# Optimization experiments

Hardware: AMD Instinct MI355X
Metric: run time of the kernel (lower is better)

## Reference

```python
import jax, jax.numpy as jnp
import numpy as np

B, NQ, ISIZE = 8, 2048, 1024
H, D, NA = 8, 128, 8            # num_head, attn_dim, num_anchor
AH = H * D                      # ahsize = 1024
ASZ = NA * D                    # anchor_size = 1024
FH = 4096                       # _fhsize
ISZ_NET = FH * H // NA          # 4096, input dim of self.net
EPS = 1e-6


def setup_inputs() -> dict:
    key = jax.random.key(0)
    ks = jax.random.split(key, 12)
    def u(k, shape, fan_in):
        s = 1.0 / np.sqrt(fan_in)
        return jax.random.uniform(k, shape, jnp.float32, -s, s)
    return {
        "inputs": jax.random.normal(ks[0], (B, NQ, ISIZE), jnp.float32),
        "ln_g": jnp.ones((ISIZE,), jnp.float32),
        "ln_b": jnp.zeros((ISIZE,), jnp.float32),
        "q_anchor": u(ks[1], (H, NA, D), D),
        "W_qkv": u(ks[2], (ISIZE, 3 * AH), ISIZE), "b_qkv": jnp.zeros((3 * AH,), jnp.float32),
        "W_an": u(ks[3], (ASZ, FH), ASZ), "b_an": jnp.zeros((FH,), jnp.float32),
        "W_n1": u(ks[4], (ISZ_NET, AH), ISZ_NET), "b_n1": jnp.zeros((AH,), jnp.float32),
        "W_n2": u(ks[5], (AH, FH), AH), "b_n2": jnp.zeros((FH,), jnp.float32),
        "W_n3": u(ks[6], (FH, AH), FH), "b_n3": jnp.zeros((AH,), jnp.float32),
        "W_k": u(ks[7], (AH, AH), AH), "b_k": jnp.zeros((AH,), jnp.float32),
        "W_o": u(ks[8], (AH, ISIZE), AH), "b_o": jnp.zeros((ISIZE,), jnp.float32),
    }


def reference(inputs, ln_g, ln_b, q_anchor, W_qkv, b_qkv, W_an, b_an,
              W_n1, b_n1, W_n2, b_n2, W_n3, b_n3, W_k, b_k, W_o, b_o):
    b, nq = inputs.shape[:2]
    scale = 1.0 / np.sqrt(D)
    # pre-LayerNorm
    mu = jnp.mean(inputs, -1, keepdims=True)
    var = jnp.mean(jnp.square(inputs - mu), -1, keepdims=True)
    x = (inputs - mu) * jax.lax.rsqrt(var + EPS) * ln_g + ln_b
    # QKV projection
    qkv = (x @ W_qkv + b_qkv).reshape(b, nq, 3, H, D)
    q = jnp.transpose(qkv[:, :, 0], (0, 2, 1, 3))   # [b,H,nq,D]
    k = qkv[:, :, 1]                                  # [b,nq,H,D]
    v = qkv[:, :, 2]                                  # [b,nq,H,D]
    # stage 1: fixed anchors attend over the sequence
    sc1 = jax.nn.softmax(jnp.einsum('had,bnhd->bhan', q_anchor, k) * scale, axis=-1)
    out = jnp.einsum('bhan,bnhd->bhad', sc1, v).reshape(b, H, ASZ)   # [b,H,NA*D]
    # anchor_net (share_head Linear + ReLU)
    out = jax.nn.relu(out @ W_an + b_an)                              # [b,H,FH]
    # regroup head-major -> anchor-major
    out = out.reshape(b, H, NA, FH // NA).transpose(0, 2, 1, 3).reshape(b, NA, ISZ_NET)
    # net: bottleneck Linear -> Linear -> ReLU -> Linear
    out = jax.nn.relu((out @ W_n1 + b_n1) @ W_n2 + b_n2) @ W_n3 + b_n3  # [b,NA,AH]
    # stage 2: queries attend over anchors
    kk = (out @ W_k + b_k).reshape(b, NA, H, D)
    sc2 = jax.nn.softmax(jnp.einsum('bhqd,bahd->bhqa', q, kk) * scale, axis=-1)
    ov = out.reshape(b, NA, H, D)
    y = jnp.einsum('bhqa,bahd->bqhd', sc2, ov).reshape(b, nq, AH)
    return y @ W_o + b_o + inputs
```

## Files before the change

### kernel.cpp

```cpp
#include <hip/hip_runtime.h>
#include <cstdint>
#include <cstddef>

typedef unsigned short u16;
typedef __attribute__((ext_vector_type(8))) short short8;
typedef __attribute__((ext_vector_type(4))) float floatx4;

__device__ __forceinline__ u16 f2bf(float f) {
  unsigned u = __float_as_uint(f);
  u += 0x7fffu + ((u >> 16) & 1u);
  return (u16)(u >> 16);
}
__device__ __forceinline__ float bf2f(u16 s) {
  return __uint_as_float(((unsigned)s) << 16);
}

__global__ __launch_bounds__(256) void ln_kernel(const float* __restrict__ x,
                                                 const float* __restrict__ g,
                                                 const float* __restrict__ bta,
                                                 u16* __restrict__ out) {
  const int row = blockIdx.x;
  const int tid = threadIdx.x;
  const float4 v = ((const float4*)(x + (size_t)row * 1024))[tid];
  float s = v.x + v.y + v.z + v.w;
#pragma unroll
  for (int o = 32; o > 0; o >>= 1) s += __shfl_down(s, o);
  __shared__ float red[4], red2[4];
  const int wv = tid >> 6, ln = tid & 63;
  if (ln == 0) red[wv] = s;
  __syncthreads();
  const float mean = (red[0] + red[1] + red[2] + red[3]) * (1.0f / 1024.0f);
  const float dx = v.x - mean, dy = v.y - mean, dz = v.z - mean, dw = v.w - mean;
  float s2 = dx * dx + dy * dy + dz * dz + dw * dw;
#pragma unroll
  for (int o = 32; o > 0; o >>= 1) s2 += __shfl_down(s2, o);
  if (ln == 0) red2[wv] = s2;
  __syncthreads();
  const float var = (red2[0] + red2[1] + red2[2] + red2[3]) * (1.0f / 1024.0f);
  const float rstd = rsqrtf(var + 1e-6f);
  const float4 gg = ((const float4*)g)[tid];
  const float4 bb = ((const float4*)bta)[tid];
  ushort4 o4;
  o4.x = f2bf(dx * rstd * gg.x + bb.x);
  o4.y = f2bf(dy * rstd * gg.y + bb.y);
  o4.z = f2bf(dz * rstd * gg.z + bb.z);
  o4.w = f2bf(dw * rstd * gg.w + bb.w);
  ((ushort4*)(out + (size_t)row * 1024))[tid] = o4;
}

__global__ __launch_bounds__(256) void transpose_bf16(const float* __restrict__ W,
                                                      u16* __restrict__ WT,
                                                      int K, int N) {
  __shared__ float t[32][33];
  const int kb = blockIdx.x * 32, nb = blockIdx.y * 32;
  const int tx = threadIdx.x & 31, ty = threadIdx.x >> 5;
#pragma unroll
  for (int i = ty; i < 32; i += 8) t[i][tx] = W[(size_t)(kb + i) * N + nb + tx];
  __syncthreads();
#pragma unroll
  for (int i = ty; i < 32; i += 8) WT[(size_t)(nb + i) * K + kb + tx] = f2bf(t[tx][i]);
}

template <int EPI>
__global__ __launch_bounds__(256) void gemm_bf16(const u16* __restrict__ A,
                                                 const u16* __restrict__ BT,
                                                 const float* __restrict__ bias,
                                                 const float* __restrict__ extra,
                                                 u16* __restrict__ outB,
                                                 float* __restrict__ outF,
                                                 int M, int N, int K) {
  __shared__ u16 sA[128 * 64];
  __shared__ u16 sB[128 * 64];
  const int tid = threadIdx.x;
  const int wave = tid >> 6, lane = tid & 63;
  const int m0 = blockIdx.x * 128, n0 = blockIdx.y * 128;
  const int wm = (wave >> 1) * 64, wn = (wave & 1) * 64;

  floatx4 acc[4][4];
  const floatx4 zero = {0.f, 0.f, 0.f, 0.f};
#pragma unroll
  for (int i = 0; i < 4; ++i)
#pragma unroll
    for (int j = 0; j < 4; ++j) acc[i][j] = zero;

  const int srow = wave * 32 + (lane >> 3);
  const int sslot = lane & 7;

  for (int kt = 0; kt < K; kt += 64) {
#pragma unroll
    for (int i = 0; i < 4; ++i) {
      const int rl = srow + i * 8;
      const int gA = sslot ^ (rl & 7);
      const u16* ga = A + (size_t)(m0 + rl) * K + kt + gA * 8;
      u16* la = sA + (wave * 32 + i * 8) * 64;
      __builtin_amdgcn_global_load_lds((const __attribute__((address_space(1))) void*)ga,
                                       (__attribute__((address_space(3))) void*)la, 16, 0, 0);
    }
#pragma unroll
    for (int i = 0; i < 4; ++i) {
      const int rl = srow + i * 8;
      const int gB = sslot ^ (rl & 7);
      const u16* gb = BT + (size_t)(n0 + rl) * K + kt + gB * 8;
      u16* lb = sB + (wave * 32 + i * 8) * 64;
      __builtin_amdgcn_global_load_lds((const __attribute__((address_space(1))) void*)gb,
                                       (__attribute__((address_space(3))) void*)lb, 16, 0, 0);
    }
    __syncthreads();
    const int fr = lane & 15, fq = lane >> 4;
#pragma unroll
    for (int ks = 0; ks < 2; ++ks) {
      short8 af[4], bfr[4];
#pragma unroll
      for (int i = 0; i < 4; ++i) {
        const int rl = wm + i * 16 + fr;
        const int g = ks * 4 + fq;
        af[i] = *(const short8*)(sA + rl * 64 + (g ^ (rl & 7)) * 8);
      }
#pragma unroll
      for (int j = 0; j < 4; ++j) {
        const int rl = wn + j * 16 + fr;
        const int g = ks * 4 + fq;
        bfr[j] = *(const short8*)(sB + rl * 64 + (g ^ (rl & 7)) * 8);
      }
#pragma unroll
      for (int i = 0; i < 4; ++i)
#pragma unroll
        for (int j = 0; j < 4; ++j)
          acc[i][j] = __builtin_amdgcn_mfma_f32_16x16x32_bf16(af[i], bfr[j], acc[i][j], 0, 0, 0);
    }
    __syncthreads();
  }

  const int fr = lane & 15, fq = lane >> 4;
#pragma unroll
  for (int i = 0; i < 4; ++i)
#pragma unroll
    for (int j = 0; j < 4; ++j)
#pragma unroll
      for (int r = 0; r < 4; ++r) {
        const int m = m0 + wm + i * 16 + fq * 4 + r;
        const int n = n0 + wn + j * 16 + fr;
        const float v = acc[i][j][r] + bias[n];
        if (EPI == 0)
          outB[(size_t)m * N + n] = f2bf(v);
        else
          outF[(size_t)m * N + n] = v + extra[(size_t)m * N + n];
      }
}

__global__ __launch_bounds__(256) void attn1_scores(const u16* __restrict__ qkv,
                                                    const float* __restrict__ q_anchor,
                                                    float* __restrict__ S) {
  __shared__ float qa[8][128];
  const int tid = threadIdx.x;
  const int chunk = blockIdx.x & 7, bh = blockIdx.x >> 3;
  const int b = bh >> 3, h = bh & 7;
  for (int i = tid; i < 1024; i += 256) qa[i >> 7][i & 127] = q_anchor[h * 1024 + i];
  __syncthreads();
  const float scale = 0.0883883476483184f;
  const int n = chunk * 256 + tid;
  const u16* kp = qkv + (size_t)(b * 2048 + n) * 3072 + 1024 + h * 128;
  float dots[8] = {0, 0, 0, 0, 0, 0, 0, 0};
#pragma unroll 8
  for (int dd = 0; dd < 128; dd += 4) {
    const ushort4 k4 = *(const ushort4*)(kp + dd);
    const float k0 = bf2f(k4.x), k1 = bf2f(k4.y), k2 = bf2f(k4.z), k3 = bf2f(k4.w);
#pragma unroll
    for (int a = 0; a < 8; ++a) {
      const float4 q4 = *(const float4*)&qa[a][dd];
      dots[a] += q4.x * k0 + q4.y * k1 + q4.z * k2 + q4.w * k3;
    }
  }
#pragma unroll
  for (int a = 0; a < 8; ++a) S[((size_t)(bh * 8 + a)) * 2048 + n] = dots[a] * scale;
}

__global__ __launch_bounds__(256) void attn1_softmax(float* __restrict__ S) {
  const int row = blockIdx.x;
  const int tid = threadIdx.x;
  float* Sp = S + (size_t)row * 2048;
  float4 v0 = ((const float4*)Sp)[tid * 2];
  float4 v1 = ((const float4*)Sp)[tid * 2 + 1];
  float mx = fmaxf(fmaxf(fmaxf(v0.x, v0.y), fmaxf(v0.z, v0.w)),
                   fmaxf(fmaxf(v1.x, v1.y), fmaxf(v1.z, v1.w)));
#pragma unroll
  for (int o = 32; o > 0; o >>= 1) mx = fmaxf(mx, __shfl_xor(mx, o));
  __shared__ float red[4];
  const int wv = tid >> 6, ln = tid & 63;
  if (ln == 0) red[wv] = mx;
  __syncthreads();
  mx = fmaxf(fmaxf(red[0], red[1]), fmaxf(red[2], red[3]));
  v0.x = __expf(v0.x - mx); v0.y = __expf(v0.y - mx);
  v0.z = __expf(v0.z - mx); v0.w = __expf(v0.w - mx);
  v1.x = __expf(v1.x - mx); v1.y = __expf(v1.y - mx);
  v1.z = __expf(v1.z - mx); v1.w = __expf(v1.w - mx);
  float sum = v0.x + v0.y + v0.z + v0.w + v1.x + v1.y + v1.z + v1.w;
#pragma unroll
  for (int o = 32; o > 0; o >>= 1) sum += __shfl_xor(sum, o);
  __shared__ float red2[4];
  if (ln == 0) red2[wv] = sum;
  __syncthreads();
  const float inv = 1.f / (red2[0] + red2[1] + red2[2] + red2[3]);
  v0.x *= inv; v0.y *= inv; v0.z *= inv; v0.w *= inv;
  v1.x *= inv; v1.y *= inv; v1.z *= inv; v1.w *= inv;
  ((float4*)Sp)[tid * 2] = v0;
  ((float4*)Sp)[tid * 2 + 1] = v1;
}

__global__ __launch_bounds__(256) void attn1_pv(const u16* __restrict__ qkv,
                                                const float* __restrict__ S,
                                                float* __restrict__ pvpart) {
  __shared__ float P[8][256];
  const int tid = threadIdx.x;
  const int chunk = blockIdx.x & 7, bh = blockIdx.x >> 3;
  const int b = bh >> 3, h = bh & 7;
  for (int i = tid; i < 2048; i += 256) {
    const int a = i >> 8, n = i & 255;
    P[a][n] = S[((size_t)(bh * 8 + a)) * 2048 + chunk * 256 + n];
  }
  __syncthreads();
  const int d = tid & 127, half = tid >> 7;
  const int nbase = chunk * 256 + half * 128;
  const u16* vp = qkv + (size_t)(b * 2048 + nbase) * 3072 + 2048 + h * 128 + d;
  float acc[8] = {0.f};
  for (int n = 0; n < 128; n += 4) {
    const float v0 = bf2f(vp[(size_t)n * 3072]);
    const float v1 = bf2f(vp[(size_t)(n + 1) * 3072]);
    const float v2 = bf2f(vp[(size_t)(n + 2) * 3072]);
    const float v3 = bf2f(vp[(size_t)(n + 3) * 3072]);
#pragma unroll
    for (int a = 0; a < 8; ++a) {
      const float4 s4 = *(const float4*)&P[a][half * 128 + n];
      acc[a] += s4.x * v0 + s4.y * v1 + s4.z * v2 + s4.w * v3;
    }
  }
  const int split = chunk * 2 + half;
#pragma unroll
  for (int a = 0; a < 8; ++a)
    pvpart[((size_t)split * 64 + bh) * 1024 + a * 128 + d] = acc[a];
}

__global__ __launch_bounds__(256) void mlp_mfma(const float* __restrict__ A,
                                                const float* __restrict__ W,
                                                float* __restrict__ part,
                                                int K, int N, int KC) {
  __shared__ float sW[64][33];
  const int tid = threadIdx.x;
  const int lane = tid & 63, wave = tid >> 6;
  const int wm = wave * 16;
  const int n0 = blockIdx.x * 64;
  const int kbeg = blockIdx.y * KC;
  const int l15 = lane & 15, kq8 = (lane >> 4) * 8;
  const int arow = wm + l15;

  floatx4 acc[4];
  const floatx4 zero = {0.f, 0.f, 0.f, 0.f};
#pragma unroll
  for (int j = 0; j < 4; ++j) acc[j] = zero;

  for (int kc = 0; kc < KC; kc += 32) {
    const int kbase = kbeg + kc;
    __syncthreads();
#pragma unroll
    for (int p = 0; p < 8; ++p) {
      const int k = p * 4 + wave;
      sW[lane][k] = W[(size_t)(kbase + k) * N + n0 + lane];
    }
    const float* ap = A + (size_t)arow * K + kbase + kq8;
    const float4 a0 = *(const float4*)ap;
    const float4 a1 = *(const float4*)(ap + 4);
    short8 af;
    af[0] = (short)f2bf(a0.x); af[1] = (short)f2bf(a0.y);
    af[2] = (short)f2bf(a0.z); af[3] = (short)f2bf(a0.w);
    af[4] = (short)f2bf(a1.x); af[5] = (short)f2bf(a1.y);
    af[6] = (short)f2bf(a1.z); af[7] = (short)f2bf(a1.w);
    __syncthreads();
#pragma unroll
    for (int j = 0; j < 4; ++j) {
      const float* wp = &sW[j * 16 + l15][kq8];
      short8 bf;
      bf[0] = (short)f2bf(wp[0]); bf[1] = (short)f2bf(wp[1]);
      bf[2] = (short)f2bf(wp[2]); bf[3] = (short)f2bf(wp[3]);
      bf[4] = (short)f2bf(wp[4]); bf[5] = (short)f2bf(wp[5]);
      bf[6] = (short)f2bf(wp[6]); bf[7] = (short)f2bf(wp[7]);
      acc[j] = __builtin_amdgcn_mfma_f32_16x16x32_bf16(af, bf, acc[j], 0, 0, 0);
    }
  }
  const int q = lane >> 4;
#pragma unroll
  for (int j = 0; j < 4; ++j)
#pragma unroll
    for (int r = 0; r < 4; ++r) {
      const int m = wm + q * 4 + r;
      const int n = n0 + j * 16 + l15;
      part[((size_t)blockIdx.y * 64 + m) * N + n] = acc[j][r];
    }
}

__global__ __launch_bounds__(256) void mlp_reduce(const float* __restrict__ part,
                                                  const float* __restrict__ bias,
                                                  float* __restrict__ out,
                                                  int N, int nsplit, int relu, int perm) {
  const int idx = blockIdx.x * 256 + threadIdx.x;
  const int e = idx * 4;
  if (e >= 64 * N) return;
  const int row = e / N, col = e - row * N;
  float4 acc;
  if (bias) acc = *(const float4*)&bias[col];
  else { acc.x = 0.f; acc.y = 0.f; acc.z = 0.f; acc.w = 0.f; }
  for (int s = 0; s < nsplit; ++s) {
    const float4 p = *(const float4*)&part[((size_t)s * 64 + row) * N + col];
    acc.x += p.x; acc.y += p.y; acc.z += p.z; acc.w += p.w;
  }
  if (relu) {
    acc.x = fmaxf(acc.x, 0.f); acc.y = fmaxf(acc.y, 0.f);
    acc.z = fmaxf(acc.z, 0.f); acc.w = fmaxf(acc.w, 0.f);
  }
  size_t oidx;
  if (!perm) {
    oidx = (size_t)row * N + col;
  } else {
    const int b = row >> 3, h = row & 7;
    oidx = (size_t)(b * 8 + (col >> 9)) * 4096 + h * 512 + (col & 511);
  }
  *(float4*)&out[oidx] = acc;
}

__global__ __launch_bounds__(256) void attn2_kernel(const u16* __restrict__ qkv,
                                                    const float* __restrict__ kk,
                                                    const float* __restrict__ onet,
                                                    u16* __restrict__ y) {
  __shared__ float kkl[8][128];
  __shared__ float ovl[8][128];
  const int tid = threadIdx.x;
  const int chunk = blockIdx.x & 7, bh = blockIdx.x >> 3;
  const int b = bh >> 3, h = bh & 7;
  for (int i = tid; i < 1024; i += 256) {
    const int a = i >> 7, d = i & 127;
    kkl[a][d] = kk[(size_t)(b * 8 + a) * 1024 + h * 128 + d];
    ovl[a][d] = onet[(size_t)(b * 8 + a) * 1024 + h * 128 + d];
  }
  __syncthreads();
  const int n = chunk * 256 + tid;
  const u16* qp = qkv + (size_t)(b * 2048 + n) * 3072 + h * 128;
  float dots[8] = {0, 0, 0, 0, 0, 0, 0, 0};
#pragma unroll 4
  for (int dd = 0; dd < 128; dd += 4) {
    const ushort4 q4 = *(const ushort4*)(qp + dd);
    const float q0 = bf2f(q4.x), q1 = bf2f(q4.y), q2 = bf2f(q4.z), q3 = bf2f(q4.w);
#pragma unroll
    for (int a = 0; a < 8; ++a) {
      const float4 k4 = *(const float4*)&kkl[a][dd];
      dots[a] += k4.x * q0 + k4.y * q1 + k4.z * q2 + k4.w * q3;
    }
  }
  const float scale = 0.0883883476483184f;
  float mx = -1e30f;
#pragma unroll
  for (int a = 0; a < 8; ++a) {
    dots[a] *= scale;
    mx = fmaxf(mx, dots[a]);
  }
  float p[8];
  float sum = 0.f;
#pragma unroll
  for (int a = 0; a < 8; ++a) {
    p[a] = __expf(dots[a] - mx);
    sum += p[a];
  }
  const float inv = 1.f / sum;
#pragma unroll
  for (int a = 0; a < 8; ++a) p[a] *= inv;
  u16* yp = y + (size_t)(b * 2048 + n) * 1024 + h * 128;
#pragma unroll 4
  for (int dd = 0; dd < 128; dd += 4) {
    float a0 = 0, a1 = 0, a2 = 0, a3 = 0;
#pragma unroll
    for (int a = 0; a < 8; ++a) {
      const float4 o4 = *(const float4*)&ovl[a][dd];
      a0 += p[a] * o4.x;
      a1 += p[a] * o4.y;
      a2 += p[a] * o4.z;
      a3 += p[a] * o4.w;
    }
    ushort4 o;
    o.x = f2bf(a0);
    o.y = f2bf(a1);
    o.z = f2bf(a2);
    o.w = f2bf(a3);
    *(ushort4*)(yp + dd) = o;
  }
}

extern "C" void kernel_launch(void* const* d_in, const int* in_sizes, int n_in,
                              void* d_out, int out_size, void* d_ws, size_t ws_size,
                              hipStream_t stream) {
  const float* inputs = (const float*)d_in[0];
  const float* ln_g = (const float*)d_in[1];
  const float* ln_b = (const float*)d_in[2];
  const float* q_anchor = (const float*)d_in[3];
  const float* W_qkv = (const float*)d_in[4];
  const float* b_qkv = (const float*)d_in[5];
  const float* W_an = (const float*)d_in[6];
  const float* b_an = (const float*)d_in[7];
  const float* W_n1 = (const float*)d_in[8];
  const float* b_n1 = (const float*)d_in[9];
  const float* W_n2 = (const float*)d_in[10];
  const float* b_n2 = (const float*)d_in[11];
  const float* W_n3 = (const float*)d_in[12];
  const float* b_n3 = (const float*)d_in[13];
  const float* W_k = (const float*)d_in[14];
  const float* b_k = (const float*)d_in[15];
  const float* W_o = (const float*)d_in[16];
  const float* b_o = (const float*)d_in[17];
  float* out = (float*)d_out;

  char* ws = (char*)d_ws;
  u16* qkv = (u16*)(ws);
  u16* xbf = (u16*)(ws + 100663296);
  float* S = (float*)(ws + 100663296);
  float* part = (float*)(ws + 109051904);
  u16* WqkvT = (u16*)(ws + 134217728);
  u16* WoT = (u16*)(ws + 140509184);
  float* att1 = (float*)(ws + 142606336);
  float* anp = (float*)(ws + 142868480);
  float* h1 = (float*)(ws + 143917056);
  float* h2 = (float*)(ws + 144179200);
  float* onet = (float*)(ws + 145227776);
  float* kkb = (float*)(ws + 145489920);

  ln_kernel<<<16384, 256, 0, stream>>>(inputs, ln_g, ln_b, xbf);
  transpose_bf16<<<dim3(32, 96), 256, 0, stream>>>(W_qkv, WqkvT, 1024, 3072);
  transpose_bf16<<<dim3(32, 32), 256, 0, stream>>>(W_o, WoT, 1024, 1024);
  gemm_bf16<0><<<dim3(128, 24), 256, 0, stream>>>(xbf, WqkvT, b_qkv, nullptr, qkv, nullptr,
                                                  16384, 3072, 1024);
  attn1_scores<<<512, 256, 0, stream>>>(qkv, q_anchor, S);
  attn1_softmax<<<512, 256, 0, stream>>>(S);
  attn1_pv<<<512, 256, 0, stream>>>(qkv, S, part);
  mlp_reduce<<<64, 256, 0, stream>>>(part, nullptr, att1, 1024, 16, 0, 0);
  mlp_mfma<<<dim3(64, 8), 256, 0, stream>>>(att1, W_an, part, 1024, 4096, 128);
  mlp_reduce<<<256, 256, 0, stream>>>(part, b_an, anp, 4096, 8, 1, 1);
  mlp_mfma<<<dim3(16, 32), 256, 0, stream>>>(anp, W_n1, part, 4096, 1024, 128);
  mlp_reduce<<<64, 256, 0, stream>>>(part, b_n1, h1, 1024, 32, 0, 0);
  mlp_mfma<<<dim3(64, 8), 256, 0, stream>>>(h1, W_n2, part, 1024, 4096, 128);
  mlp_reduce<<<256, 256, 0, stream>>>(part, b_n2, h2, 4096, 8, 1, 0);
  mlp_mfma<<<dim3(16, 32), 256, 0, stream>>>(h2, W_n3, part, 4096, 1024, 128);
  mlp_reduce<<<64, 256, 0, stream>>>(part, b_n3, onet, 1024, 32, 0, 0);
  mlp_mfma<<<dim3(16, 16), 256, 0, stream>>>(onet, W_k, part, 1024, 1024, 64);
  mlp_reduce<<<64, 256, 0, stream>>>(part, b_k, kkb, 1024, 16, 0, 0);
  attn2_kernel<<<512, 256, 0, stream>>>(qkv, kkb, onet, xbf);
  gemm_bf16<1><<<dim3(128, 8), 256, 0, stream>>>(xbf, WoT, b_o, inputs, nullptr, out,
                                                 16384, 1024, 1024);
}
```

Before: 637.4 us.

## Rewrite bf16 GEMM as 256x256 double-buffered ping-pong pipeline with 8 waves

Replaces the simple 128x128 single-buffered GEMM with a 256x256 tile, 512-thread kernel that double-buffers LDS. It splits each K-step into four quadrant phases, interleaving global-to-LDS prefetch of the next tiles with MFMA work. It uses s_setprio and explicit waitcnt/barriers to overlap loads and compute and to raise arithmetic intensity per block. The risks are higher register and LDS pressure (128KB LDS), fewer blocks for the N=1024 output GEMM, and subtle synchronisation correctness in the hand-scheduled phases.

```diff
diff --git a/kernel.cpp b/kernel.cpp
--- a/kernel.cpp
+++ b/kernel.cpp
@@ -61,91 +61,167 @@
   for (int i = ty; i < 32; i += 8) WT[(size_t)(nb + i) * K + kb + tx] = f2bf(t[tx][i]);
 }
 
+
+__device__ __forceinline__ void stage2(const u16* __restrict__ src, u16* dst,
+                                       int growbase, int kcol, int ld,
+                                       int wave, int lane) {
+#pragma unroll
+  for (int i = 0; i < 2; ++i) {
+    const int row = (i * 8 + wave) * 8 + (lane >> 3);
+    const u16* gp = src + (size_t)(growbase + row) * ld + kcol + (((lane & 7) ^ (row & 7)) << 3);
+    u16* lp = dst + (i * 8 + wave) * 512;
+    __builtin_amdgcn_global_load_lds((const __attribute__((address_space(1))) void*)gp,
+                                     (__attribute__((address_space(3))) void*)lp, 16, 0, 0);
+  }
+}
+
+__device__ __forceinline__ void rdA4(short8 (&af)[4][2], const u16* sbuf, int half,
+                                     int wr, int fr, int fq) {
+#pragma unroll
+  for (int mi = 0; mi < 4; ++mi)
+#pragma unroll
+    for (int ks = 0; ks < 2; ++ks) {
+      const int row = half * 128 + wr * 64 + mi * 16 + fr;
+      const int kg = ks * 4 + fq;
+      af[mi][ks] = *(const short8*)(sbuf + row * 64 + ((kg ^ (row & 7)) << 3));
+    }
+}
+
+__device__ __forceinline__ void rdB2(short8 (&bfr)[2][2], const u16* sbuf, int half,
+                                     int wc, int fr, int fq) {
+#pragma unroll
+  for (int ni = 0; ni < 2; ++ni)
+#pragma unroll
+    for (int ks = 0; ks < 2; ++ks) {
+      const int row = half * 128 + wc * 32 + ni * 16 + fr;
+      const int kg = ks * 4 + fq;
+      bfr[ni][ks] = *(const short8*)(sbuf + row * 64 + ((kg ^ (row & 7)) << 3));
+    }
+}
+
+template <int Q>
+__device__ __forceinline__ void mfmaQ(floatx4 (&acc)[4][4][2], const short8 (&af)[4][2],
+                                      const short8 (&bfr)[2][2]) {
+#pragma unroll
+  for (int mi = 0; mi < 4; ++mi)
+#pragma unroll
+    for (int ni = 0; ni < 2; ++ni) {
+      acc[Q][mi][ni] = __builtin_amdgcn_mfma_f32_16x16x32_bf16(af[mi][0], bfr[ni][0], acc[Q][mi][ni], 0, 0, 0);
+      acc[Q][mi][ni] = __builtin_amdgcn_mfma_f32_16x16x32_bf16(af[mi][1], bfr[ni][1], acc[Q][mi][ni], 0, 0, 0);
+    }
+}
+
+__device__ __forceinline__ void phase_pre() {
+  __builtin_amdgcn_s_barrier();
+  asm volatile("s_waitcnt lgkmcnt(0)" ::: "memory");
+  __builtin_amdgcn_sched_barrier(0);
+  __builtin_amdgcn_s_setprio(1);
+}
+__device__ __forceinline__ void phase_post() {
+  __builtin_amdgcn_s_setprio(0);
+  __builtin_amdgcn_s_barrier();
+}
+
+template <int B_>
+__device__ __forceinline__ void gtile(int t, int NT, int K,
+                                      u16 (&sA)[2][16384], u16 (&sB)[2][16384],
+                                      const u16* __restrict__ A, const u16* __restrict__ BT,
+                                      int m0, int n0, int wave, int lane,
+                                      int wr, int wc, int fr, int fq,
+                                      short8 (&af)[4][2], short8 (&bfr)[2][2],
+                                      floatx4 (&acc)[4][4][2]) {
+  rdA4(af, sA[B_], 0, wr, fr, fq);
+  rdB2(bfr, sB[B_], 0, wc, fr, fq);
+  if (t + 1 < NT) stage2(A, &sA[B_ ^ 1][8192], m0 + 128, (t + 1) << 6, K, wave, lane);
+  phase_pre();
+  mfmaQ<0>(acc, af, bfr);
+  phase_post();
+  rdB2(bfr, sB[B_], 1, wc, fr, fq);
+  if (t + 1 < NT) stage2(BT, &sB[B_ ^ 1][0], n0, (t + 1) << 6, K, wave, lane);
+  phase_pre();
+  mfmaQ<1>(acc, af, bfr);
+  phase_post();
+  rdA4(af, sA[B_], 1, wr, fr, fq);
+  if (t + 2 < NT) stage2(A, &sA[B_][0], m0, (t + 2) << 6, K, wave, lane);
+  phase_pre();
+  mfmaQ<2>(acc, af, bfr);
+  phase_post();
+  rdB2(bfr, sB[B_], 0, wc, fr, fq);
+  if (t + 2 < NT) stage2(BT, &sB[B_][8192], n0 + 128, (t + 2) << 6, K, wave, lane);
+  __builtin_amdgcn_s_barrier();
+  asm volatile("s_waitcnt lgkmcnt(0)" ::: "memory");
+  __builtin_amdgcn_sched_barrier(0);
+  __builtin_amdgcn_s_setprio(1);
+  mfmaQ<3>(acc, af, bfr);
+  __builtin_amdgcn_s_setprio(0);
+  if (t + 2 < NT) {
+    asm volatile("s_waitcnt vmcnt(4)" ::: "memory");
+  } else {
+    asm volatile("s_waitcnt vmcnt(0)" ::: "memory");
+  }
+  __builtin_amdgcn_s_barrier();
+}
+
 template <int EPI>
-__global__ __launch_bounds__(256) void gemm_bf16(const u16* __restrict__ A,
-                                                 const u16* __restrict__ BT,
-                                                 const float* __restrict__ bias,
-                                                 const float* __restrict__ extra,
-                                                 u16* __restrict__ outB,
-                                                 float* __restrict__ outF,
-                                                 int M, int N, int K) {
-  __shared__ u16 sA[128 * 64];
-  __shared__ u16 sB[128 * 64];
+__global__ __launch_bounds__(512, 2) void gemm_bf16(const u16* __restrict__ A,
+                                                    const u16* __restrict__ BT,
+                                                    const float* __restrict__ bias,
+                                                    const float* __restrict__ extra,
+                                                    u16* __restrict__ outB,
+                                                    float* __restrict__ outF,
+                                                    int M, int N, int K) {
+  __shared__ u16 sA[2][16384];
+  __shared__ u16 sB[2][16384];
   const int tid = threadIdx.x;
   const int wave = tid >> 6, lane = tid & 63;
-  const int m0 = blockIdx.x * 128, n0 = blockIdx.y * 128;
-  const int wm = (wave >> 1) * 64, wn = (wave & 1) * 64;
-
-  floatx4 acc[4][4];
+  const int m0 = blockIdx.x * 256, n0 = blockIdx.y * 256;
+  const int wr = wave >> 2, wc = wave & 3;
+  const int fr = lane & 15, fq = lane >> 4;
+  const int NT = K >> 6;
+
+  floatx4 acc[4][4][2];
   const floatx4 zero = {0.f, 0.f, 0.f, 0.f};
 #pragma unroll
-  for (int i = 0; i < 4; ++i)
-#pragma unroll
-    for (int j = 0; j < 4; ++j) acc[i][j] = zero;
-
-  const int srow = wave * 32 + (lane >> 3);
-  const int sslot = lane & 7;
-
-  for (int kt = 0; kt < K; kt += 64) {
-#pragma unroll
-    for (int i = 0; i < 4; ++i) {
-      const int rl = srow + i * 8;
-      const int gA = sslot ^ (rl & 7);
-      const u16* ga = A + (size_t)(m0 + rl) * K + kt + gA * 8;
-      u16* la = sA + (wave * 32 + i * 8) * 64;
-      __builtin_amdgcn_global_load_lds((const __attribute__((address_space(1))) void*)ga,
-                                       (__attribute__((address_space(3))) void*)la, 16, 0, 0);
-    }
-#pragma unroll
-    for (int i = 0; i < 4; ++i) {
-      const int rl = srow + i * 8;
-      const int gB = sslot ^ (rl & 7);
-      const u16* gb = BT + (size_t)(n0 + rl) * K + kt + gB * 8;
-      u16* lb = sB + (wave * 32 + i * 8) * 64;
-      __builtin_amdgcn_global_load_lds((const __attribute__((address_space(1))) void*)gb,
-                                       (__attribute__((address_space(3))) void*)lb, 16, 0, 0);
-    }
-    __syncthreads();
-    const int fr = lane & 15, fq = lane >> 4;
-#pragma unroll
-    for (int ks = 0; ks < 2; ++ks) {
-      short8 af[4], bfr[4];
-#pragma unroll
-      for (int i = 0; i < 4; ++i) {
-        const int rl = wm + i * 16 + fr;
-        const int g = ks * 4 + fq;
-        af[i] = *(const short8*)(sA + rl * 64 + (g ^ (rl & 7)) * 8);
-      }
-#pragma unroll
-      for (int j = 0; j < 4; ++j) {
-        const int rl = wn + j * 16 + fr;
-        const int g = ks * 4 + fq;
-        bfr[j] = *(const short8*)(sB + rl * 64 + (g ^ (rl & 7)) * 8);
-      }
-#pragma unroll
-      for (int i = 0; i < 4; ++i)
-#pragma unroll
-        for (int j = 0; j < 4; ++j)
-          acc[i][j] = __builtin_amdgcn_mfma_f32_16x16x32_bf16(af[i], bfr[j], acc[i][j], 0, 0, 0);
-    }
-    __syncthreads();
-  }
-
-  const int fr = lane & 15, fq = lane >> 4;
-#pragma unroll
-  for (int i = 0; i < 4; ++i)
-#pragma unroll
-    for (int j = 0; j < 4; ++j)
-#pragma unroll
-      for (int r = 0; r < 4; ++r) {
-        const int m = m0 + wm + i * 16 + fq * 4 + r;
-        const int n = n0 + wn + j * 16 + fr;
-        const float v = acc[i][j][r] + bias[n];
-        if (EPI == 0)
-          outB[(size_t)m * N + n] = f2bf(v);
-        else
-          outF[(size_t)m * N + n] = v + extra[(size_t)m * N + n];
-      }
+  for (int q = 0; q < 4; ++q)
+#pragma unroll
+    for (int i = 0; i < 4; ++i)
+#pragma unroll
+      for (int j = 0; j < 2; ++j) acc[q][i][j] = zero;
+
+  short8 af[4][2], bfr[2][2];
+
+  stage2(A, &sA[0][0], m0, 0, K, wave, lane);
+  stage2(A, &sA[0][8192], m0 + 128, 0, K, wave, lane);
+  stage2(BT, &sB[0][0], n0, 0, K, wave, lane);
+  stage2(BT, &sB[0][8192], n0 + 128, 0, K, wave, lane);
+  stage2(A, &sA[1][0], m0, 64, K, wave, lane);
+  stage2(BT, &sB[1][8192], n0 + 128, 64, K, wave, lane);
+  asm volatile("s_waitcnt vmcnt(4)" ::: "memory");
+  __builtin_amdgcn_s_barrier();
+
+  for (int t = 0; t < NT; t += 2) {
+    gtile<0>(t, NT, K, sA, sB, A, BT, m0, n0, wave, lane, wr, wc, fr, fq, af, bfr, acc);
+    gtile<1>(t + 1, NT, K, sA, sB, A, BT, m0, n0, wave, lane, wr, wc, fr, fq, af, bfr, acc);
+  }
+
+#pragma unroll
+  for (int q = 0; q < 4; ++q) {
+    const int QM = q >> 1, QN = QM ^ (q & 1);
+#pragma unroll
+    for (int mi = 0; mi < 4; ++mi)
+#pragma unroll
+      for (int ni = 0; ni < 2; ++ni)
+#pragma unroll
+        for (int r = 0; r < 4; ++r) {
+          const int m = m0 + QM * 128 + wr * 64 + mi * 16 + fq * 4 + r;
+          const int n = n0 + QN * 128 + wc * 32 + ni * 16 + fr;
+          const float v = acc[q][mi][ni][r] + bias[n];
+          if (EPI == 0)
+            outB[(size_t)m * N + n] = f2bf(v);
+          else
+            outF[(size_t)m * N + n] = v + extra[(size_t)m * N + n];
+        }
+  }
 }
 
 __global__ __launch_bounds__(256) void attn1_scores(const u16* __restrict__ qkv,
@@ -432,8 +508,8 @@
   ln_kernel<<<16384, 256, 0, stream>>>(inputs, ln_g, ln_b, xbf);
   transpose_bf16<<<dim3(32, 96), 256, 0, stream>>>(W_qkv, WqkvT, 1024, 3072);
   transpose_bf16<<<dim3(32, 32), 256, 0, stream>>>(W_o, WoT, 1024, 1024);
-  gemm_bf16<0><<<dim3(128, 24), 256, 0, stream>>>(xbf, WqkvT, b_qkv, nullptr, qkv, nullptr,
-                                                  16384, 3072, 1024);
+  gemm_bf16<0><<<dim3(64, 12), 512, 0, stream>>>(xbf, WqkvT, b_qkv, nullptr, qkv, nullptr,
+                                                 16384, 3072, 1024);
   attn1_scores<<<512, 256, 0, stream>>>(qkv, q_anchor, S);
   attn1_softmax<<<512, 256, 0, stream>>>(S);
   attn1_pv<<<512, 256, 0, stream>>>(qkv, S, part);
@@ -449,6 +525,6 @@
   mlp_mfma<<<dim3(16, 16), 256, 0, stream>>>(onet, W_k, part, 1024, 1024, 64);
   mlp_reduce<<<64, 256, 0, stream>>>(part, b_k, kkb, 1024, 16, 0, 0);
   attn2_kernel<<<512, 256, 0, stream>>>(qkv, kkb, onet, xbf);
-  gemm_bf16<1><<<dim3(128, 8), 256, 0, stream>>>(xbf, WoT, b_o, inputs, nullptr, out,
-                                                 16384, 1024, 1024);
-}
+  gemm_bf16<1><<<dim3(64, 4), 512, 0, stream>>>(xbf, WoT, b_o, inputs, nullptr, out,
+                                                16384, 1024, 1024);
+}
```

After: 597.6 us. -6.2%, faster.
